# Optimization experiments

Measured on AMD Instinct MI355X. Metric: run time of the kernel, lower is better.

Reference implementation:

```python
import jax, jax.numpy as jnp
import numpy as np

NQ, DEPTH = 4, 2
C64 = jnp.complex64


def _ry(theta):
    # theta: scalar or (B,) -> (...,2,2) complex
    h = theta.astype(jnp.float32) / 2
    c, s = jnp.cos(h).astype(C64), jnp.sin(h).astype(C64)
    return jnp.stack([jnp.stack([c, -s], -1), jnp.stack([s, c], -1)], -2)


def _rot(phi, theta, omega):
    # PennyLane Rot = RZ(omega) @ RY(theta) @ RZ(phi), scalars -> (2,2) complex
    h = theta / 2
    c, s = jnp.cos(h), jnp.sin(h)
    ep = jnp.exp(-0.5j * (phi + omega).astype(C64))
    em = jnp.exp(0.5j * (phi - omega).astype(C64))
    return jnp.array(1.0, C64) * jnp.stack([
        jnp.stack([ep * c, -em * s], -1),
        jnp.stack([jnp.conj(em) * s, jnp.conj(ep) * c], -1)], -2)


def _apply_1q(state, U, wire):
    # state: (B,2,2,2,2); U: (2,2) or (B,2,2)
    s = jnp.moveaxis(state, wire + 1, -1)
    if U.ndim == 2:
        s = jnp.einsum('ij,bklmj->bklmi', U, s)
    else:
        s = jnp.einsum('bij,bklmj->bklmi', U, s)
    return jnp.moveaxis(s, -1, wire + 1)


def _cnot(state, ctrl, tgt):
    s = jnp.moveaxis(state, [ctrl + 1, tgt + 1], [-2, -1])
    s = s.at[..., 1, :].set(s[..., 1, ::-1])
    return jnp.moveaxis(s, [-2, -1], [ctrl + 1, tgt + 1])


def _circuit(x, q_weights):
    B = x.shape[0]
    state = jnp.zeros((B, 2, 2, 2, 2), C64).at[:, 0, 0, 0, 0].set(1.0)
    # angle encoding: RY(x[:, w]) on wire w (batched gates)
    for w in range(NQ):
        state = _apply_1q(state, _ry(x[:, w]), w)
    # variational layers
    for layer in range(DEPTH):
        for w in range(NQ):
            U = _rot(q_weights[layer, w, 0], q_weights[layer, w, 1], q_weights[layer, w, 2])
            state = _apply_1q(state, U, w)
        for w in range(NQ - 1):
            state = _cnot(state, w, w + 1)
        state = _cnot(state, NQ - 1, 0)  # num_qubits > 2 wrap-around
    # expval PauliZ on each wire
    probs = jnp.abs(state) ** 2  # (B,2,2,2,2) float32
    z = jnp.array([1.0, -1.0], jnp.float32)
    outs = [jnp.einsum('bijkl,' + 'ijkl'[w] + '->b', probs, z) for w in range(NQ)]
    return jnp.stack(outs, axis=1).astype(x.dtype)  # (B, 4)


def setup_inputs() -> dict:
    key = jax.random.key(0)
    k1, k2 = jax.random.split(key)
    B = 2_000_000
    x = jax.random.uniform(k1, (B, NQ), jnp.float32, minval=0.0, maxval=np.pi)
    q_weights = jax.random.normal(k2, (DEPTH, NQ, 3), jnp.float32) * 0.01
    return {"x": x, "q_weights": q_weights}


def reference(x, q_weights):
    return _circuit(x, q_weights)
```

## Files before the change

### kernel.cpp

```cpp
#include <hip/hip_runtime.h>

#define NQ 4
#define DEPTH 2
#define BLK 256
#define K 4

typedef float v2f __attribute__((ext_vector_type(2)));
typedef float v4f __attribute__((ext_vector_type(4)));

__device__ __forceinline__ void pk_fma_lo(v2f& acc, v2f u, v2f b) {
    asm("v_pk_fma_f32 %0, %1, %2, %0 op_sel:[0,0,0] op_sel_hi:[0,1,1]"
        : "+v"(acc) : "v"(u), "v"(b));
}
__device__ __forceinline__ void pk_fma_hi(v2f& acc, v2f u, v2f b) {
    asm("v_pk_fma_f32 %0, %1, %2, %0 op_sel:[1,0,0] op_sel_hi:[1,1,1]"
        : "+v"(acc) : "v"(u), "v"(b));
}
__device__ __forceinline__ v2f pk_mul(v2f a, v2f b) {
    v2f d;
    asm("v_pk_mul_f32 %0, %1, %2" : "=v"(d) : "v"(a), "v"(b));
    return d;
}
__device__ __forceinline__ void pk_fma(v2f& acc, v2f a, v2f b) {
    asm("v_pk_fma_f32 %0, %1, %2, %0" : "+v"(acc) : "v"(a), "v"(b));
}

__device__ __forceinline__ float2 cmul(float2 a, float2 b) {
    return make_float2(a.x * b.x - a.y * b.y, a.x * b.y + a.y * b.x);
}
__device__ __forceinline__ float2 cadd(float2 a, float2 b) {
    return make_float2(a.x + b.x, a.y + b.y);
}

__device__ __forceinline__ void build_u_col(const float* __restrict__ qw, int col,
                                            float2 amp[16]) {
#pragma unroll
    for (int i = 0; i < 16; i++)
        amp[i] = make_float2((i == col) ? 1.f : 0.f, 0.f);

#pragma unroll
    for (int layer = 0; layer < DEPTH; layer++) {
#pragma unroll
        for (int w = 0; w < NQ; w++) {
            const float* g = qw + (layer * NQ + w) * 3;
            float phi = g[0], theta = g[1], omega = g[2];
            float ch, sh, sp, cp, sm, cm;
            __sincosf(0.5f * theta, &sh, &ch);
            __sincosf(-0.5f * (phi + omega), &sp, &cp);
            __sincosf(0.5f * (phi - omega), &sm, &cm);
            float2 U00 = make_float2(cp * ch, sp * ch);
            float2 U01 = make_float2(-cm * sh, -sm * sh);
            float2 U10 = make_float2(cm * sh, -sm * sh);
            float2 U11 = make_float2(cp * ch, -sp * ch);
            const int mask = 8 >> w;
#pragma unroll
            for (int i0 = 0; i0 < 16; i0++) {
                if (i0 & mask) continue;
                const int i1 = i0 | mask;
                float2 a0 = amp[i0], a1 = amp[i1];
                amp[i0] = cadd(cmul(U00, a0), cmul(U01, a1));
                amp[i1] = cadd(cmul(U10, a0), cmul(U11, a1));
            }
        }
#pragma unroll
        for (int c = 0; c < NQ; c++) {
            const int t = (c + 1) & 3;
            const int cmsk = 8 >> c, tmsk = 8 >> t;
#pragma unroll
            for (int i = 0; i < 16; i++) {
                if ((i & cmsk) && !(i & tmsk)) {
                    float2 tmp = amp[i];
                    amp[i] = amp[i | tmsk];
                    amp[i | tmsk] = tmp;
                }
            }
        }
    }
}

__global__ void build_u_kernel(const float* __restrict__ qw, v2f* __restrict__ Ug) {
    const int tid = threadIdx.x;
    if (tid < 16) {
        float2 amp[16];
        build_u_col(qw, tid, amp);
#pragma unroll
        for (int i = 0; i < 16; i++) {
            v2f u; u.x = amp[i].x; u.y = amp[i].y;
            Ug[i * 16 + tid] = u;
        }
    }
}

__device__ __forceinline__ void vqc_main_body(const float* __restrict__ x,
                                              const v4f* UmS,
                                              float* __restrict__ out, int B) {
    const int tid = threadIdx.x;
    const int base = blockIdx.x * (BLK * K) + tid;

    float4 xv[K];
    bool val[K];
#pragma unroll
    for (int k = 0; k < K; k++) {
        const int b = base + k * BLK;
        val[k] = (b < B);
        xv[k] = val[k] ? ((const float4*)x)[b] : make_float4(0.f, 0.f, 0.f, 0.f);
    }

    const float R = 0.07957747154594767f;
    float a01[K][4], a23[K][4];
#pragma unroll
    for (int k = 0; k < K; k++) {
        float s0 = __builtin_amdgcn_sinf(xv[k].x * R), c0 = __builtin_amdgcn_cosf(xv[k].x * R);
        float s1 = __builtin_amdgcn_sinf(xv[k].y * R), c1 = __builtin_amdgcn_cosf(xv[k].y * R);
        float s2 = __builtin_amdgcn_sinf(xv[k].z * R), c2 = __builtin_amdgcn_cosf(xv[k].z * R);
        float s3 = __builtin_amdgcn_sinf(xv[k].w * R), c3 = __builtin_amdgcn_cosf(xv[k].w * R);
        a01[k][0] = c0 * c1; a01[k][1] = c0 * s1; a01[k][2] = s0 * c1; a01[k][3] = s0 * s1;
        a23[k][0] = c2 * c3; a23[k][1] = c2 * s3; a23[k][2] = s2 * c3; a23[k][3] = s2 * s3;
    }
    v2f a01p[2][4], a23p[2][4];
#pragma unroll
    for (int p = 0; p < 2; p++)
#pragma unroll
        for (int i = 0; i < 4; i++) {
            v2f t0; t0.x = a01[2 * p][i]; t0.y = a01[2 * p + 1][i]; a01p[p][i] = t0;
            v2f t1; t1.x = a23[2 * p][i]; t1.y = a23[2 * p + 1][i]; a23p[p][i] = t1;
        }

    v2f ow[4][2];
#pragma unroll
    for (int w = 0; w < 4; w++)
#pragma unroll
        for (int p = 0; p < 2; p++) ow[w][p] = (v2f)0.f;

#pragma unroll 1
    for (int iq = 0; iq < 4; iq++) {
        const v4f* rowp = UmS + iq * 32;
        v2f accre[4][2], accim[4][2];
#pragma unroll
        for (int ii = 0; ii < 4; ii++)
#pragma unroll
            for (int p = 0; p < 2; p++) { accre[ii][p] = (v2f)0.f; accim[ii][p] = (v2f)0.f; }

#pragma unroll
        for (int jp = 0; jp < 8; jp++) {
            const int j0 = 2 * jp, j1 = 2 * jp + 1;
            v2f ps0[2], ps1[2];
#pragma unroll
            for (int p = 0; p < 2; p++) {
                ps0[p] = pk_mul(a01p[p][j0 >> 2], a23p[p][j0 & 3]);
                ps1[p] = pk_mul(a01p[p][j1 >> 2], a23p[p][j1 & 3]);
            }
#pragma unroll
            for (int ii = 0; ii < 4; ii++) {
                v4f q = rowp[ii * 8 + jp];
                v2f u0 = __builtin_shufflevector(q, q, 0, 1);
                v2f u1 = __builtin_shufflevector(q, q, 2, 3);
#pragma unroll
                for (int p = 0; p < 2; p++) {
                    pk_fma_lo(accre[ii][p], u0, ps0[p]);
                    pk_fma_hi(accim[ii][p], u0, ps0[p]);
                    pk_fma_lo(accre[ii][p], u1, ps1[p]);
                    pk_fma_hi(accim[ii][p], u1, ps1[p]);
                }
            }
        }

#pragma unroll
        for (int p = 0; p < 2; p++) {
            v2f p0 = pk_mul(accre[0][p], accre[0][p]); pk_fma(p0, accim[0][p], accim[0][p]);
            v2f p1 = pk_mul(accre[1][p], accre[1][p]); pk_fma(p1, accim[1][p], accim[1][p]);
            v2f p2 = pk_mul(accre[2][p], accre[2][p]); pk_fma(p2, accim[2][p], accim[2][p]);
            v2f p3 = pk_mul(accre[3][p], accre[3][p]); pk_fma(p3, accim[3][p], accim[3][p]);
            v2f s01 = p0 + p1, d01 = p0 - p1;
            v2f s23 = p2 + p3, d23 = p2 - p3;
            v2f ssum = s01 + s23;
            ow[2][p] += s01 - s23;
            ow[3][p] += d01 + d23;
            if (iq & 2) ow[0][p] -= ssum; else ow[0][p] += ssum;
            if (iq & 1) ow[1][p] -= ssum; else ow[1][p] += ssum;
        }
    }

#pragma unroll
    for (int p = 0; p < 2; p++)
#pragma unroll
        for (int e = 0; e < 2; e++) {
            const int k = 2 * p + e;
            const int b = base + k * BLK;
            if (val[k]) {
                float4 o;
                o.x = (e == 0) ? ow[0][p].x : ow[0][p].y;
                o.y = (e == 0) ? ow[1][p].x : ow[1][p].y;
                o.z = (e == 0) ? ow[2][p].x : ow[2][p].y;
                o.w = (e == 0) ? ow[3][p].x : ow[3][p].y;
                ((float4*)out)[b] = o;
            }
        }
}

__global__ __launch_bounds__(BLK, 4) void vqc_main(const float* __restrict__ x,
                                                   const v4f* __restrict__ Ug,
                                                   float* __restrict__ out, int B) {
    __shared__ v4f UmS[128];
    if (threadIdx.x < 128) UmS[threadIdx.x] = Ug[threadIdx.x];
    __syncthreads();
    vqc_main_body(x, UmS, out, B);
}

__global__ void vqc_fused(const float* __restrict__ x, const float* __restrict__ qw,
                          float* __restrict__ out, int B) {
    __shared__ v4f UmS[128];
    if (threadIdx.x < 16) {
        float2 amp[16];
        build_u_col(qw, threadIdx.x, amp);
        v2f* Um2 = (v2f*)UmS;
#pragma unroll
        for (int i = 0; i < 16; i++) {
            v2f u; u.x = amp[i].x; u.y = amp[i].y;
            Um2[i * 16 + threadIdx.x] = u;
        }
    }
    __syncthreads();
    vqc_main_body(x, UmS, out, B);
}

extern "C" void kernel_launch(void* const* d_in, const int* in_sizes, int n_in,
                              void* d_out, int out_size, void* d_ws, size_t ws_size,
                              hipStream_t stream) {
    const float* x  = (const float*)d_in[0];
    const float* qw = (const float*)d_in[1];
    float* out = (float*)d_out;
    const int B = in_sizes[0] / NQ;
    const int blocks = (B + BLK * K - 1) / (BLK * K);

    if (ws_size >= 256 * sizeof(v2f)) {
        v2f* Ug = (v2f*)d_ws;
        build_u_kernel<<<1, 64, 0, stream>>>(qw, Ug);
        vqc_main<<<blocks, BLK, 0, stream>>>(x, (const v4f*)Ug, out, B);
    } else {
        vqc_fused<<<blocks, BLK, 0, stream>>>(x, qw, out, B);
    }
}
```

Baseline: 110.1 us.

## Feed unitary coefficients as scalar operands from global instead of LDS

The main kernel no longer stages the 16x16 unitary in LDS. It reads the coefficients directly from the global workspace with wave-uniform indices, so the compiler can use scalar loads, and the inline packed FMAs now take the coefficient through an SGPR constraint. The aim is to drop the LDS staging, the barrier and the per-lane LDS reads from the inner loop. The risk lies in the fused fallback path, which still passes an LDS pointer: it is not uniform in SGPRs, so the 's' constraint may force readfirstlane copies or fail to compile. Scalar load latency and the dropped occupancy hint in launch bounds may also change the schedule.

```diff
diff --git a/kernel.cpp b/kernel.cpp
--- a/kernel.cpp
+++ b/kernel.cpp
@@ -8,13 +8,13 @@
 typedef float v2f __attribute__((ext_vector_type(2)));
 typedef float v4f __attribute__((ext_vector_type(4)));
 
-__device__ __forceinline__ void pk_fma_lo(v2f& acc, v2f u, v2f b) {
+__device__ __forceinline__ void pk_fma_lo_s(v2f& acc, v2f u, v2f b) {
     asm("v_pk_fma_f32 %0, %1, %2, %0 op_sel:[0,0,0] op_sel_hi:[0,1,1]"
-        : "+v"(acc) : "v"(u), "v"(b));
-}
-__device__ __forceinline__ void pk_fma_hi(v2f& acc, v2f u, v2f b) {
+        : "+v"(acc) : "s"(u), "v"(b));
+}
+__device__ __forceinline__ void pk_fma_hi_s(v2f& acc, v2f u, v2f b) {
     asm("v_pk_fma_f32 %0, %1, %2, %0 op_sel:[1,0,0] op_sel_hi:[1,1,1]"
-        : "+v"(acc) : "v"(u), "v"(b));
+        : "+v"(acc) : "s"(u), "v"(b));
 }
 __device__ __forceinline__ v2f pk_mul(v2f a, v2f b) {
     v2f d;
@@ -91,8 +91,9 @@
     }
 }
 
+template <typename UPtr>
 __device__ __forceinline__ void vqc_main_body(const float* __restrict__ x,
-                                              const v4f* UmS,
+                                              UPtr U,
                                               float* __restrict__ out, int B) {
     const int tid = threadIdx.x;
     const int base = blockIdx.x * (BLK * K) + tid;
@@ -134,7 +135,6 @@
 
 #pragma unroll 1
     for (int iq = 0; iq < 4; iq++) {
-        const v4f* rowp = UmS + iq * 32;
         v2f accre[4][2], accim[4][2];
 #pragma unroll
         for (int ii = 0; ii < 4; ii++)
@@ -142,26 +142,16 @@
             for (int p = 0; p < 2; p++) { accre[ii][p] = (v2f)0.f; accim[ii][p] = (v2f)0.f; }
 
 #pragma unroll
-        for (int jp = 0; jp < 8; jp++) {
-            const int j0 = 2 * jp, j1 = 2 * jp + 1;
-            v2f ps0[2], ps1[2];
-#pragma unroll
-            for (int p = 0; p < 2; p++) {
-                ps0[p] = pk_mul(a01p[p][j0 >> 2], a23p[p][j0 & 3]);
-                ps1[p] = pk_mul(a01p[p][j1 >> 2], a23p[p][j1 & 3]);
-            }
+        for (int j = 0; j < 16; j++) {
+            v2f ps0 = pk_mul(a01p[0][j >> 2], a23p[0][j & 3]);
+            v2f ps1 = pk_mul(a01p[1][j >> 2], a23p[1][j & 3]);
 #pragma unroll
             for (int ii = 0; ii < 4; ii++) {
-                v4f q = rowp[ii * 8 + jp];
-                v2f u0 = __builtin_shufflevector(q, q, 0, 1);
-                v2f u1 = __builtin_shufflevector(q, q, 2, 3);
-#pragma unroll
-                for (int p = 0; p < 2; p++) {
-                    pk_fma_lo(accre[ii][p], u0, ps0[p]);
-                    pk_fma_hi(accim[ii][p], u0, ps0[p]);
-                    pk_fma_lo(accre[ii][p], u1, ps1[p]);
-                    pk_fma_hi(accim[ii][p], u1, ps1[p]);
-                }
+                const v2f u = U[(iq * 4 + ii) * 16 + j];
+                pk_fma_lo_s(accre[ii][0], u, ps0);
+                pk_fma_hi_s(accim[ii][0], u, ps0);
+                pk_fma_lo_s(accre[ii][1], u, ps1);
+                pk_fma_hi_s(accim[ii][1], u, ps1);
             }
         }
 
@@ -198,30 +188,26 @@
         }
 }
 
-__global__ __launch_bounds__(BLK, 4) void vqc_main(const float* __restrict__ x,
-                                                   const v4f* __restrict__ Ug,
-                                                   float* __restrict__ out, int B) {
-    __shared__ v4f UmS[128];
-    if (threadIdx.x < 128) UmS[threadIdx.x] = Ug[threadIdx.x];
-    __syncthreads();
-    vqc_main_body(x, UmS, out, B);
+__global__ __launch_bounds__(BLK) void vqc_main(const float* __restrict__ x,
+                                                const v2f* __restrict__ Ug,
+                                                float* __restrict__ out, int B) {
+    vqc_main_body(x, Ug, out, B);
 }
 
 __global__ void vqc_fused(const float* __restrict__ x, const float* __restrict__ qw,
                           float* __restrict__ out, int B) {
-    __shared__ v4f UmS[128];
+    __shared__ v2f Um[256];
     if (threadIdx.x < 16) {
         float2 amp[16];
         build_u_col(qw, threadIdx.x, amp);
-        v2f* Um2 = (v2f*)UmS;
 #pragma unroll
         for (int i = 0; i < 16; i++) {
             v2f u; u.x = amp[i].x; u.y = amp[i].y;
-            Um2[i * 16 + threadIdx.x] = u;
+            Um[i * 16 + threadIdx.x] = u;
         }
     }
     __syncthreads();
-    vqc_main_body(x, UmS, out, B);
+    vqc_main_body(x, (const v2f*)Um, out, B);
 }
 
 extern "C" void kernel_launch(void* const* d_in, const int* in_sizes, int n_in,
@@ -236,7 +222,7 @@
     if (ws_size >= 256 * sizeof(v2f)) {
         v2f* Ug = (v2f*)d_ws;
         build_u_kernel<<<1, 64, 0, stream>>>(qw, Ug);
-        vqc_main<<<blocks, BLK, 0, stream>>>(x, (const v4f*)Ug, out, B);
+        vqc_main<<<blocks, BLK, 0, stream>>>(x, Ug, out, B);
     } else {
         vqc_fused<<<blocks, BLK, 0, stream>>>(x, qw, out, B);
     }
```

Measured after the change: 107.3 us. -2.5%, faster.
